# Optimization experiments

Measured on AMD Instinct MI355X. Metric: run time of the kernel, lower is better.

## Reference

```python
import jax, jax.numpy as jnp
import numpy as np

B, C, W, H, Z = 2, 32, 96, 96, 64
IC = C  # inter_channels defaults to in_channels (required by depthwise g conv)
THRESH = 1.5
EPS = 1e-5


def setup_inputs() -> dict:
    key = jax.random.key(0)
    ks = jax.random.split(key, 12)
    s1 = 1.0 / np.sqrt(C)   # 1x1x1 conv fan-in
    s3 = 1.0 / np.sqrt(3.0) # depthwise (1,1,3) conv fan-in per channel
    return {
        "x": jax.random.normal(ks[0], (B, C, W, H, Z), jnp.float32),
        # per-sample spacings in [0,3): mixes both branches around thresh 1.5
        "spacings": jax.random.uniform(ks[1], (B, 3), jnp.float32) * 3.0,
        "theta_w": jax.random.normal(ks[2], (IC, C), jnp.float32) * s1,
        "theta_b": jax.random.normal(ks[3], (IC,), jnp.float32) * s1,
        "phi_w": jax.random.normal(ks[4], (IC, C), jnp.float32) * s1,
        "phi_b": jax.random.normal(ks[5], (IC,), jnp.float32) * s1,
        "g_w": jax.random.normal(ks[6], (C, 3), jnp.float32) * s3,   # depthwise kernel along z
        "g_b": jax.random.normal(ks[7], (C,), jnp.float32) * s3,
        "W_w": jax.random.normal(ks[8], (C, IC), jnp.float32) * s1,
        "W_b": jax.random.normal(ks[9], (C,), jnp.float32) * s1,
        # torch inits BN gamma=0, beta=0 (zero-init residual trick); use small random
        "bn_gamma": jax.random.normal(ks[10], (C,), jnp.float32) * 0.1,
        "bn_beta": jax.random.normal(ks[11], (C,), jnp.float32) * 0.1,
    }


def _cvec(v):
    return v.reshape(1, -1, 1, 1, 1)


def _conv1x1(h, w, b):
    # 1x1x1 Conv3d == channel-mixing matmul
    return jnp.einsum('bcwhz,oc->bowhz', h, w) + _cvec(b)


def reference(x, spacings, theta_w, theta_b, phi_w, phi_b, g_w, g_b, W_w, W_b, bn_gamma, bn_beta):
    # theta/phi: 1x1x1 convs -> (B, IC, W, H, Z)
    t = _conv1x1(x, theta_w, theta_b)
    p = _conv1x1(x, phi_w, phi_b)

    # g: depthwise conv along z, kernel 3, pad 1 (groups=C)
    xp = jnp.pad(x, ((0, 0), (0, 0), (0, 0), (0, 0), (1, 1)))
    gx = (xp[..., :-2] * _cvec(g_w[:, 0])
          + xp[..., 1:-1] * _cvec(g_w[:, 1])
          + xp[..., 2:] * _cvec(g_w[:, 2])
          + _cvec(g_b))

    # non-local attention along z per (b, w, h) row: scores (B, W, H, Z, Z)
    f = jnp.einsum('bcwhz,bcwhy->bwhzy', t, p)
    a = jax.nn.softmax(f, axis=-1)
    y = jnp.einsum('bwhzy,bcwhy->bcwhz', a, gx)
    nl = y + x  # residual inside compute_x

    # per-sample branch on z-spacing, vectorized with where
    mask = (spacings[:, -1] <= THRESH).reshape(-1, 1, 1, 1, 1)
    res = jnp.where(mask, nl, x)

    # W: 1x1x1 conv + BatchNorm3d (training-mode batch stats)
    out = _conv1x1(res, W_w, W_b)
    mean = jnp.mean(out, axis=(0, 2, 3, 4), keepdims=True)
    var = jnp.var(out, axis=(0, 2, 3, 4), keepdims=True)
    out = (out - mean) * jax.lax.rsqrt(var + EPS)
    return out * _cvec(bn_gamma) + _cvec(bn_beta)
```

## Files before the change

kernel.cpp:

```cpp
#include <hip/hip_runtime.h>
#include <stdint.h>

#define CHS 589824
#define ROWS 18432
#define WHn 9216
#define NRED 1179648.0f
#define LOG2E 1.4426950408889634f

typedef short s16x8 __attribute__((ext_vector_type(8)));
typedef float f32x4v __attribute__((ext_vector_type(4)));

#define MFMA16 __builtin_amdgcn_mfma_f32_16x16x32_bf16

#define WSFRAG 10240

#define OXH 0
#define OP  8704
#define OG  13312
#define LDSZ 17664

static __device__ __forceinline__ uint16_t bfh(float v) {
    union { __bf16 h; uint16_t u; } c; c.h = (__bf16)v; return c.u;
}
static __device__ __forceinline__ float bf2f(uint16_t u) {
    union { uint32_t x; float f; } c; c.x = (uint32_t)u << 16; return c.f;
}
static __device__ __forceinline__ uint32_t pk2u(uint16_t a, uint16_t b) {
    return (uint32_t)a | ((uint32_t)b << 16);
}
static __device__ __forceinline__ uint32_t pkbf(float a, float b) {
    return pk2u(bfh(a), bfh(b));
}
static __device__ __forceinline__ float ex2(float x) {
    float r;
    asm("v_exp_f32 %0, %1" : "=v"(r) : "v"(x));
    return r;
}
static __device__ __forceinline__ s16x8 rd8(const char* p) {
    union { uint64_t q[2]; s16x8 s; } v;
    v.q[0] = *(const uint64_t*)p;
    v.q[1] = *(const uint64_t*)(p + 8);
    return v.s;
}

static __device__ __forceinline__ void wfrag2(const float* __restrict__ Wp, int mt, int l15, int kb,
                                              float sc, s16x8& hi, s16x8& lo) {
    const float* p = Wp + (l15 + 16*mt)*32 + 8*kb;
    const float4 f0 = *(const float4*)p;
    const float4 f1 = *(const float4*)(p + 4);
    float f[8] = {f0.x*sc, f0.y*sc, f0.z*sc, f0.w*sc, f1.x*sc, f1.y*sc, f1.z*sc, f1.w*sc};
    union { uint32_t u[4]; s16x8 v; } rh, rl;
    #pragma unroll
    for (int i = 0; i < 4; ++i) {
        const uint16_t h0 = bfh(f[2*i]), h1 = bfh(f[2*i+1]);
        rh.u[i] = pk2u(h0, h1);
        rl.u[i] = pk2u(bfh(f[2*i] - bf2f(h0)), bfh(f[2*i+1] - bf2f(h1)));
    }
    hi = rh.v; lo = rl.v;
}
static __device__ __forceinline__ s16x8 wfragW(const float* __restrict__ Wp, int mt, int l15, int kb) {
    const float* p = Wp + (l15 + 16*mt)*32;
    const float4 f0 = *(const float4*)(p + 4*kb);
    const float4 f1 = *(const float4*)(p + 16 + 4*kb);
    union { uint32_t u[4]; s16x8 v; } r;
    r.u[0] = pkbf(f0.x, f0.y); r.u[1] = pkbf(f0.z, f0.w);
    r.u[2] = pkbf(f1.x, f1.y); r.u[3] = pkbf(f1.z, f1.w);
    return r.v;
}

__global__ __launch_bounds__(256) void k0_frag(
    const float* __restrict__ theta_w, const float* __restrict__ phi_w,
    const float* __restrict__ Ww, char* __restrict__ ws)
{
    const int tid = threadIdx.x;
    const int m = tid >> 7;
    const int r = tid & 127;
    const int mt = r >> 6, l = r & 63;
    s16x8 hi, lo;
    wfrag2(m ? phi_w : theta_w, mt, l & 15, l >> 4, m ? 1.0f : LOG2E, hi, lo);
    *(s16x8*)(ws + m*4096 + (mt*64 + l)*16)        = hi;
    *(s16x8*)(ws + m*4096 + 2048 + (mt*64 + l)*16) = lo;
    if (tid < 128) {
        const int mtw = tid >> 6, lw = tid & 63;
        *(s16x8*)(ws + 8192 + (mtw*64 + lw)*16) = wfragW(Ww, mtw, lw & 15, lw >> 4);
    }
}

__global__ __launch_bounds__(128, 4) void k1_row(
    const float* __restrict__ x, const float* __restrict__ spacings,
    const float* __restrict__ theta_b, const float* __restrict__ phi_b,
    const float* __restrict__ g_w, const float* __restrict__ g_b,
    const float* __restrict__ Wb, const char* __restrict__ frags,
    float* __restrict__ out, float* __restrict__ part)
{
    __shared__ __align__(16) char lds[LDSZ];
    const int t = threadIdx.x;
    const int wv = t >> 6, l = t & 63;
    const int l15 = l & 15, kb = l >> 4;
    const int row = blockIdx.x;
    const int b = row / WHn, wh = row - b*WHn;
    const long base = (long)b*32*CHS + (long)wh*64;

    float xv[16];
    {
        const float* xp = x + base;
        #pragma unroll
        for (int j = 0; j < 16; ++j) xv[j] = xp[(long)(16*wv + j)*CHS + l];
    }
    {
        #pragma unroll
        for (int j = 0; j < 8; ++j) {
            const int c0 = 16*wv + 2*j;
            const uint16_t h0 = bfh(xv[2*j]), h1 = bfh(xv[2*j+1]);
            *(uint32_t*)(lds + OXH + l*136 + c0*2)      = pk2u(h0, h1);
            *(uint32_t*)(lds + OXH + l*136 + 64 + c0*2) =
                pk2u(bfh(xv[2*j] - bf2f(h0)), bfh(xv[2*j+1] - bf2f(h1)));
        }
        const int pG = 32*(l >> 5) + 8*((l >> 2) & 3) + 4*((l >> 4) & 1) + (l & 3);
        #pragma unroll
        for (int j = 0; j < 16; ++j) {
            const int c = 16*wv + j;
            float xm = __shfl_up(xv[j], 1);    if (l == 0)  xm = 0.f;
            float xp2 = __shfl_down(xv[j], 1); if (l == 63) xp2 = 0.f;
            const float g = g_w[3*c]*xm + g_w[3*c+1]*xv[j] + g_w[3*c+2]*xp2 + g_b[c];
            *(uint16_t*)(lds + OG + c*136 + 2*pG) = bfh(g);
        }
    }
    __syncthreads();

    s16x8 bth[2], btl[2];
    {
        s16x8 bxh[2], bxl[2];
        #pragma unroll
        for (int nt = 0; nt < 2; ++nt) {
            const int zr = 32*wv + 16*nt + l15;
            bxh[nt] = rd8(lds + OXH + zr*136 + 16*kb);
            bxl[nt] = rd8(lds + OXH + zr*136 + 64 + 16*kb);
        }
        {
            const s16x8 t0h = *(const s16x8*)(frags + l*16);
            const s16x8 t1h = *(const s16x8*)(frags + 1024 + l*16);
            const s16x8 t0l = *(const s16x8*)(frags + 2048 + l*16);
            const s16x8 t1l = *(const s16x8*)(frags + 3072 + l*16);
            const float4 b0 = *(const float4*)(theta_b + 4*kb);
            const float4 b1 = *(const float4*)(theta_b + 16 + 4*kb);
            #pragma unroll
            for (int nt = 0; nt < 2; ++nt) {
                f32x4v T0; T0[0]=b0.x*LOG2E; T0[1]=b0.y*LOG2E; T0[2]=b0.z*LOG2E; T0[3]=b0.w*LOG2E;
                f32x4v T1; T1[0]=b1.x*LOG2E; T1[1]=b1.y*LOG2E; T1[2]=b1.z*LOG2E; T1[3]=b1.w*LOG2E;
                T0 = MFMA16(t0h, bxh[nt], T0, 0, 0, 0);
                T0 = MFMA16(t0h, bxl[nt], T0, 0, 0, 0);
                T0 = MFMA16(t0l, bxh[nt], T0, 0, 0, 0);
                T1 = MFMA16(t1h, bxh[nt], T1, 0, 0, 0);
                T1 = MFMA16(t1h, bxl[nt], T1, 0, 0, 0);
                T1 = MFMA16(t1l, bxh[nt], T1, 0, 0, 0);
                uint16_t h[8];
                #pragma unroll
                for (int r = 0; r < 4; ++r) { h[r] = bfh(T0[r]); h[4+r] = bfh(T1[r]); }
                union { uint32_t u[4]; s16x8 s; } H, L2;
                H.u[0] = pk2u(h[0], h[1]); H.u[1] = pk2u(h[2], h[3]);
                H.u[2] = pk2u(h[4], h[5]); H.u[3] = pk2u(h[6], h[7]);
                L2.u[0] = pkbf(T0[0]-bf2f(h[0]), T0[1]-bf2f(h[1]));
                L2.u[1] = pkbf(T0[2]-bf2f(h[2]), T0[3]-bf2f(h[3]));
                L2.u[2] = pkbf(T1[0]-bf2f(h[4]), T1[1]-bf2f(h[5]));
                L2.u[3] = pkbf(T1[2]-bf2f(h[6]), T1[3]-bf2f(h[7]));
                bth[nt] = H.s; btl[nt] = L2.s;
            }
        }
        {
            const s16x8 p0h = *(const s16x8*)(frags + 4096 + l*16);
            const s16x8 p1h = *(const s16x8*)(frags + 4096 + 1024 + l*16);
            const s16x8 p0l = *(const s16x8*)(frags + 4096 + 2048 + l*16);
            const s16x8 p1l = *(const s16x8*)(frags + 4096 + 3072 + l*16);
            const float4 c0 = *(const float4*)(phi_b + 4*kb);
            const float4 c1 = *(const float4*)(phi_b + 16 + 4*kb);
            #pragma unroll
            for (int nt = 0; nt < 2; ++nt) {
                const int zr = 32*wv + 16*nt + l15;
                f32x4v P0; P0[0]=c0.x; P0[1]=c0.y; P0[2]=c0.z; P0[3]=c0.w;
                f32x4v P1; P1[0]=c1.x; P1[1]=c1.y; P1[2]=c1.z; P1[3]=c1.w;
                P0 = MFMA16(p0h, bxh[nt], P0, 0, 0, 0);
                P0 = MFMA16(p0h, bxl[nt], P0, 0, 0, 0);
                P0 = MFMA16(p0l, bxh[nt], P0, 0, 0, 0);
                P1 = MFMA16(p1h, bxh[nt], P1, 0, 0, 0);
                P1 = MFMA16(p1h, bxl[nt], P1, 0, 0, 0);
                P1 = MFMA16(p1l, bxh[nt], P1, 0, 0, 0);
                union { uint32_t u[2]; uint64_t q; } w;
                w.u[0] = pkbf(P0[0], P0[1]); w.u[1] = pkbf(P0[2], P0[3]);
                *(uint64_t*)(lds + OP + zr*72 + 16*kb) = w.q;
                w.u[0] = pkbf(P1[0], P1[1]); w.u[1] = pkbf(P1[2], P1[3]);
                *(uint64_t*)(lds + OP + zr*72 + 16*kb + 8) = w.q;
            }
        }
    }
    __syncthreads();

    f32x4v Fq[2][4];
    __builtin_amdgcn_s_setprio(1);
    #pragma unroll
    for (int yt = 0; yt < 4; ++yt) {
        const s16x8 pah = rd8(lds + OP + (16*yt + l15)*72 + 16*kb);
        #pragma unroll
        for (int nt = 0; nt < 2; ++nt) {
            f32x4v zz; zz[0]=0.f; zz[1]=0.f; zz[2]=0.f; zz[3]=0.f;
            zz = MFMA16(pah, bth[nt], zz, 0, 0, 0);
            zz = MFMA16(pah, btl[nt], zz, 0, 0, 0);
            Fq[nt][yt] = zz;
        }
    }
    __builtin_amdgcn_s_setprio(0);

    s16x8 apk[2][2];
    float inv[2];
    #pragma unroll
    for (int nt = 0; nt < 2; ++nt) {
        float mx = -3.4e38f;
        #pragma unroll
        for (int yt = 0; yt < 4; ++yt)
            #pragma unroll
            for (int r = 0; r < 4; ++r) mx = fmaxf(mx, Fq[nt][yt][r]);
        mx = fmaxf(mx, __shfl_xor(mx, 16));
        mx = fmaxf(mx, __shfl_xor(mx, 32));
        float p[4][4]; float sum = 0.f;
        #pragma unroll
        for (int yt = 0; yt < 4; ++yt)
            #pragma unroll
            for (int r = 0; r < 4; ++r) { p[yt][r] = ex2(Fq[nt][yt][r] - mx); sum += p[yt][r]; }
        sum += __shfl_xor(sum, 16);
        sum += __shfl_xor(sum, 32);
        inv[nt] = 1.0f / sum;
        #pragma unroll
        for (int ks = 0; ks < 2; ++ks) {
            union { uint32_t u[4]; s16x8 s; } A;
            A.u[0] = pkbf(p[2*ks][0],   p[2*ks][1]);
            A.u[1] = pkbf(p[2*ks][2],   p[2*ks][3]);
            A.u[2] = pkbf(p[2*ks+1][0], p[2*ks+1][1]);
            A.u[3] = pkbf(p[2*ks+1][2], p[2*ks+1][3]);
            apk[nt][ks] = A.s;
        }
    }

    const bool msk = spacings[b*3 + 2] <= 1.5f;
    s16x8 brf[2];
    #pragma unroll
    for (int nt = 0; nt < 2; ++nt) {
        const int zr = 32*wv + 16*nt + l15;
        f32x4v Yq[2];
        #pragma unroll
        for (int r = 0; r < 4; ++r) { Yq[0][r] = 0.f; Yq[1][r] = 0.f; }
        __builtin_amdgcn_s_setprio(1);
        #pragma unroll
        for (int ks = 0; ks < 2; ++ks) {
            #pragma unroll
            for (int mt = 0; mt < 2; ++mt) {
                const s16x8 gA = rd8(lds + OG + (16*mt + l15)*136 + 64*ks + 16*kb);
                Yq[mt] = MFMA16(gA, apk[nt][ks], Yq[mt], 0, 0, 0);
            }
        }
        __builtin_amdgcn_s_setprio(0);
        union { uint32_t u[4]; s16x8 s; } R;
        #pragma unroll
        for (int mt = 0; mt < 2; ++mt) {
            const uint64_t xh = *(const uint64_t*)(lds + OXH + zr*136 + (16*mt + 4*kb)*2);
            float rv[4];
            #pragma unroll
            for (int r = 0; r < 4; ++r) {
                const float xr = bf2f((uint16_t)(xh >> (16*r)));
                rv[r] = msk ? fmaf(Yq[mt][r], inv[nt], xr) : xr;
            }
            R.u[2*mt]   = pkbf(rv[0], rv[1]);
            R.u[2*mt+1] = pkbf(rv[2], rv[3]);
        }
        brf[nt] = R.s;
    }

    {
        const s16x8 aW0 = *(const s16x8*)(frags + 8192 + l*16);
        const s16x8 aW1 = *(const s16x8*)(frags + 8192 + (64 + l)*16);
        const float4 wb0 = *(const float4*)(Wb + 4*kb);
        const float4 wb1 = *(const float4*)(Wb + 16 + 4*kb);
        #pragma unroll
        for (int nt = 0; nt < 2; ++nt) {
            const int zr = 32*wv + 16*nt + l15;
            f32x4v accs[2];
            f32x4v a0; a0[0]=wb0.x; a0[1]=wb0.y; a0[2]=wb0.z; a0[3]=wb0.w;
            f32x4v a1; a1[0]=wb1.x; a1[1]=wb1.y; a1[2]=wb1.z; a1[3]=wb1.w;
            __builtin_amdgcn_s_setprio(1);
            accs[0] = MFMA16(aW0, brf[nt], a0, 0, 0, 0);
            accs[1] = MFMA16(aW1, brf[nt], a1, 0, 0, 0);
            __builtin_amdgcn_s_setprio(0);
            float* op = out + base + zr;
            #pragma unroll
            for (int mt = 0; mt < 2; ++mt)
                #pragma unroll
                for (int r = 0; r < 4; ++r)
                    op[(long)(16*mt + 4*kb + r)*CHS] = accs[mt][r];
            const int sr = row*4 + 2*wv + nt;
            float bs[8];
            #pragma unroll
            for (int mt = 0; mt < 2; ++mt)
                #pragma unroll
                for (int r = 0; r < 4; ++r) bs[4*mt+r] = accs[mt][r];
            #pragma unroll
            for (int off = 1; off < 16; off <<= 1)
                #pragma unroll
                for (int i = 0; i < 8; ++i) bs[i] += __shfl_xor(bs[i], off);
            if (l15 == 0) {
                #pragma unroll
                for (int mt = 0; mt < 2; ++mt)
                    #pragma unroll
                    for (int r = 0; r < 4; ++r)
                        part[sr*64 + 16*mt + 4*kb + r] = bs[4*mt+r];
            }
            #pragma unroll
            for (int mt = 0; mt < 2; ++mt)
                #pragma unroll
                for (int r = 0; r < 4; ++r) { const float v = accs[mt][r]; bs[4*mt+r] = v*v; }
            #pragma unroll
            for (int off = 1; off < 16; off <<= 1)
                #pragma unroll
                for (int i = 0; i < 8; ++i) bs[i] += __shfl_xor(bs[i], off);
            if (l15 == 0) {
                #pragma unroll
                for (int mt = 0; mt < 2; ++mt)
                    #pragma unroll
                    for (int r = 0; r < 4; ++r)
                        part[sr*64 + 32 + 16*mt + 4*kb + r] = bs[4*mt+r];
            }
        }
    }
}

__global__ __launch_bounds__(256) void k2a(const float* __restrict__ part,
                                           float* __restrict__ part2)
{
    __shared__ float red[4][64];
    const int t = threadIdx.x, lane = t & 63, grp = t >> 6;
    const int p = blockIdx.x;
    float s = 0.f;
    for (int k = 0; k < 72; ++k) s += part[(p*288 + grp + 4*k)*64 + lane];
    red[grp][lane] = s;
    __syncthreads();
    if (t < 64) part2[p*64 + t] = red[0][t] + red[1][t] + red[2][t] + red[3][t];
}

__global__ __launch_bounds__(256) void k2b(const float* __restrict__ part2,
    const float* __restrict__ gamma, const float* __restrict__ beta,
    float* __restrict__ sc)
{
    __shared__ float red[4][64];
    __shared__ float tot[64];
    const int t = threadIdx.x, lane = t & 63, grp = t >> 6;
    float s = 0.f;
    for (int k = 0; k < 64; ++k) s += part2[(grp + 4*k)*64 + lane];
    red[grp][lane] = s;
    __syncthreads();
    if (t < 64) tot[t] = red[0][t] + red[1][t] + red[2][t] + red[3][t];
    __syncthreads();
    if (t < 32) {
        const float mean = tot[t] / NRED;
        const float var  = tot[32+t] / NRED - mean*mean;
        const float rstd = rsqrtf(var + 1e-5f);
        const float scale = gamma[t] * rstd;
        sc[t]    = scale;
        sc[32+t] = fmaf(-mean, scale, beta[t]);
    }
}

__global__ __launch_bounds__(256) void k3_norm(float* __restrict__ out,
                                               const float* __restrict__ sc)
{
    __shared__ float s[64];
    if (threadIdx.x < 64) s[threadIdx.x] = sc[threadIdx.x];
    __syncthreads();
    const int total4 = 2*32*CHS/4;
    const int Q = CHS/4;
    for (int i = blockIdx.x*256 + threadIdx.x; i < total4; i += gridDim.x*256) {
        float4 v = ((const float4*)out)[i];
        const int c = (i / Q) & 31;
        const float scale = s[c], shift = s[32+c];
        v.x = fmaf(v.x, scale, shift);
        v.y = fmaf(v.y, scale, shift);
        v.z = fmaf(v.z, scale, shift);
        v.w = fmaf(v.w, scale, shift);
        ((float4*)out)[i] = v;
    }
}

extern "C" void kernel_launch(void* const* d_in, const int* in_sizes, int n_in,
                              void* d_out, int out_size, void* d_ws, size_t ws_size,
                              hipStream_t stream) {
    const float* x        = (const float*)d_in[0];
    const float* spacings = (const float*)d_in[1];
    const float* theta_w  = (const float*)d_in[2];
    const float* theta_b  = (const float*)d_in[3];
    const float* phi_w    = (const float*)d_in[4];
    const float* phi_b    = (const float*)d_in[5];
    const float* g_w      = (const float*)d_in[6];
    const float* g_b      = (const float*)d_in[7];
    const float* Ww       = (const float*)d_in[8];
    const float* Wb       = (const float*)d_in[9];
    const float* gamma    = (const float*)d_in[10];
    const float* beta     = (const float*)d_in[11];
    float* out   = (float*)d_out;
    char*  frags = (char*)d_ws;
    float* part  = (float*)((char*)d_ws + WSFRAG);
    float* part2 = part + (size_t)ROWS*256;
    float* sc    = part2 + 256*64;

    hipLaunchKernelGGL(k0_frag, dim3(1), dim3(256), 0, stream, theta_w, phi_w, Ww, frags);
    hipLaunchKernelGGL(k1_row, dim3(ROWS), dim3(128), 0, stream,
                       x, spacings, theta_b, phi_b, g_w, g_b, Wb, frags, out, part);
    hipLaunchKernelGGL(k2a, dim3(256), dim3(256), 0, stream, part, part2);
    hipLaunchKernelGGL(k2b, dim3(1), dim3(256), 0, stream, part2, gamma, beta, sc);
    hipLaunchKernelGGL(k3_norm, dim3(4096), dim3(256), 0, stream, out, sc);
}
```

Baseline: 171.8 us.

## Process two rows per block and prefetch the next row's input during compute

The row kernel now handles two consecutive (w,h) rows per block, halving the grid. It loads the second row's x values into registers after the first row's projection stage, so the global load overlaps with the score, softmax and output MFMA work. Per-block setup such as reading the spacing mask is amortized over both rows. The cost is higher register pressure from the extra 16-float buffer, which could reduce occupancy under the (128,4) launch bounds, plus an added barrier between iterations.

```diff
diff --git a/kernel.cpp b/kernel.cpp
--- a/kernel.cpp
+++ b/kernel.cpp
@@ -97,235 +97,243 @@
     const int t = threadIdx.x;
     const int wv = t >> 6, l = t & 63;
     const int l15 = l & 15, kb = l >> 4;
-    const int row = blockIdx.x;
-    const int b = row / WHn, wh = row - b*WHn;
+    const int row0 = blockIdx.x*2;
+    const int b = row0 / WHn, wh = row0 - b*WHn;
     const long base = (long)b*32*CHS + (long)wh*64;
-
-    float xv[16];
-    {
-        const float* xp = x + base;
+    const bool msk = spacings[b*3 + 2] <= 1.5f;
+
+    float xv[2][16];
+    #pragma unroll
+    for (int j = 0; j < 16; ++j) xv[0][j] = x[base + (long)(16*wv + j)*CHS + l];
+
+    #pragma unroll
+    for (int it = 0; it < 2; ++it) {
+        {
+            #pragma unroll
+            for (int j = 0; j < 8; ++j) {
+                const int c0 = 16*wv + 2*j;
+                const uint16_t h0 = bfh(xv[it][2*j]), h1 = bfh(xv[it][2*j+1]);
+                *(uint32_t*)(lds + OXH + l*136 + c0*2)      = pk2u(h0, h1);
+                *(uint32_t*)(lds + OXH + l*136 + 64 + c0*2) =
+                    pk2u(bfh(xv[it][2*j] - bf2f(h0)), bfh(xv[it][2*j+1] - bf2f(h1)));
+            }
+            const int pG = 32*(l >> 5) + 8*((l >> 2) & 3) + 4*((l >> 4) & 1) + (l & 3);
+            #pragma unroll
+            for (int j = 0; j < 16; ++j) {
+                const int c = 16*wv + j;
+                float xm = __shfl_up(xv[it][j], 1);    if (l == 0)  xm = 0.f;
+                float xp2 = __shfl_down(xv[it][j], 1); if (l == 63) xp2 = 0.f;
+                const float g = g_w[3*c]*xm + g_w[3*c+1]*xv[it][j] + g_w[3*c+2]*xp2 + g_b[c];
+                *(uint16_t*)(lds + OG + c*136 + 2*pG) = bfh(g);
+            }
+        }
+        __syncthreads();
+
+        s16x8 bth[2], btl[2];
+        {
+            s16x8 bxh[2], bxl[2];
+            #pragma unroll
+            for (int nt = 0; nt < 2; ++nt) {
+                const int zr = 32*wv + 16*nt + l15;
+                bxh[nt] = rd8(lds + OXH + zr*136 + 16*kb);
+                bxl[nt] = rd8(lds + OXH + zr*136 + 64 + 16*kb);
+            }
+            {
+                const s16x8 t0h = *(const s16x8*)(frags + l*16);
+                const s16x8 t1h = *(const s16x8*)(frags + 1024 + l*16);
+                const s16x8 t0l = *(const s16x8*)(frags + 2048 + l*16);
+                const s16x8 t1l = *(const s16x8*)(frags + 3072 + l*16);
+                const float4 b0 = *(const float4*)(theta_b + 4*kb);
+                const float4 b1 = *(const float4*)(theta_b + 16 + 4*kb);
+                #pragma unroll
+                for (int nt = 0; nt < 2; ++nt) {
+                    f32x4v T0; T0[0]=b0.x*LOG2E; T0[1]=b0.y*LOG2E; T0[2]=b0.z*LOG2E; T0[3]=b0.w*LOG2E;
+                    f32x4v T1; T1[0]=b1.x*LOG2E; T1[1]=b1.y*LOG2E; T1[2]=b1.z*LOG2E; T1[3]=b1.w*LOG2E;
+                    T0 = MFMA16(t0h, bxh[nt], T0, 0, 0, 0);
+                    T0 = MFMA16(t0h, bxl[nt], T0, 0, 0, 0);
+                    T0 = MFMA16(t0l, bxh[nt], T0, 0, 0, 0);
+                    T1 = MFMA16(t1h, bxh[nt], T1, 0, 0, 0);
+                    T1 = MFMA16(t1h, bxl[nt], T1, 0, 0, 0);
+                    T1 = MFMA16(t1l, bxh[nt], T1, 0, 0, 0);
+                    uint16_t h[8];
+                    #pragma unroll
+                    for (int r = 0; r < 4; ++r) { h[r] = bfh(T0[r]); h[4+r] = bfh(T1[r]); }
+                    union { uint32_t u[4]; s16x8 s; } H, L2;
+                    H.u[0] = pk2u(h[0], h[1]); H.u[1] = pk2u(h[2], h[3]);
+                    H.u[2] = pk2u(h[4], h[5]); H.u[3] = pk2u(h[6], h[7]);
+                    L2.u[0] = pkbf(T0[0]-bf2f(h[0]), T0[1]-bf2f(h[1]));
+                    L2.u[1] = pkbf(T0[2]-bf2f(h[2]), T0[3]-bf2f(h[3]));
+                    L2.u[2] = pkbf(T1[0]-bf2f(h[4]), T1[1]-bf2f(h[5]));
+                    L2.u[3] = pkbf(T1[2]-bf2f(h[6]), T1[3]-bf2f(h[7]));
+                    bth[nt] = H.s; btl[nt] = L2.s;
+                }
+            }
+            {
+                const s16x8 p0h = *(const s16x8*)(frags + 4096 + l*16);
+                const s16x8 p1h = *(const s16x8*)(frags + 4096 + 1024 + l*16);
+                const s16x8 p0l = *(const s16x8*)(frags + 4096 + 2048 + l*16);
+                const s16x8 p1l = *(const s16x8*)(frags + 4096 + 3072 + l*16);
+                const float4 c0 = *(const float4*)(phi_b + 4*kb);
+                const float4 c1 = *(const float4*)(phi_b + 16 + 4*kb);
+                #pragma unroll
+                for (int nt = 0; nt < 2; ++nt) {
+                    const int zr = 32*wv + 16*nt + l15;
+                    f32x4v P0; P0[0]=c0.x; P0[1]=c0.y; P0[2]=c0.z; P0[3]=c0.w;
+                    f32x4v P1; P1[0]=c1.x; P1[1]=c1.y; P1[2]=c1.z; P1[3]=c1.w;
+                    P0 = MFMA16(p0h, bxh[nt], P0, 0, 0, 0);
+                    P0 = MFMA16(p0h, bxl[nt], P0, 0, 0, 0);
+                    P0 = MFMA16(p0l, bxh[nt], P0, 0, 0, 0);
+                    P1 = MFMA16(p1h, bxh[nt], P1, 0, 0, 0);
+                    P1 = MFMA16(p1h, bxl[nt], P1, 0, 0, 0);
+                    P1 = MFMA16(p1l, bxh[nt], P1, 0, 0, 0);
+                    union { uint32_t u[2]; uint64_t q; } w;
+                    w.u[0] = pkbf(P0[0], P0[1]); w.u[1] = pkbf(P0[2], P0[3]);
+                    *(uint64_t*)(lds + OP + zr*72 + 16*kb) = w.q;
+                    w.u[0] = pkbf(P1[0], P1[1]); w.u[1] = pkbf(P1[2], P1[3]);
+                    *(uint64_t*)(lds + OP + zr*72 + 16*kb + 8) = w.q;
+                }
+            }
+        }
+        __syncthreads();
+
+        if (it == 0) {
+            #pragma unroll
+            for (int j = 0; j < 16; ++j)
+                xv[1][j] = x[base + 64 + (long)(16*wv + j)*CHS + l];
+        }
+
+        f32x4v Fq[2][4];
+        __builtin_amdgcn_s_setprio(1);
         #pragma unroll
-        for (int j = 0; j < 16; ++j) xv[j] = xp[(long)(16*wv + j)*CHS + l];
-    }
-    {
+        for (int yt = 0; yt < 4; ++yt) {
+            const s16x8 pah = rd8(lds + OP + (16*yt + l15)*72 + 16*kb);
+            #pragma unroll
+            for (int nt = 0; nt < 2; ++nt) {
+                f32x4v zz; zz[0]=0.f; zz[1]=0.f; zz[2]=0.f; zz[3]=0.f;
+                zz = MFMA16(pah, bth[nt], zz, 0, 0, 0);
+                zz = MFMA16(pah, btl[nt], zz, 0, 0, 0);
+                Fq[nt][yt] = zz;
+            }
+        }
+        __builtin_amdgcn_s_setprio(0);
+
+        s16x8 apk[2][2];
+        float inv[2];
         #pragma unroll
-        for (int j = 0; j < 8; ++j) {
-            const int c0 = 16*wv + 2*j;
-            const uint16_t h0 = bfh(xv[2*j]), h1 = bfh(xv[2*j+1]);
-            *(uint32_t*)(lds + OXH + l*136 + c0*2)      = pk2u(h0, h1);
-            *(uint32_t*)(lds + OXH + l*136 + 64 + c0*2) =
-                pk2u(bfh(xv[2*j] - bf2f(h0)), bfh(xv[2*j+1] - bf2f(h1)));
-        }
-        const int pG = 32*(l >> 5) + 8*((l >> 2) & 3) + 4*((l >> 4) & 1) + (l & 3);
-        #pragma unroll
-        for (int j = 0; j < 16; ++j) {
-            const int c = 16*wv + j;
-            float xm = __shfl_up(xv[j], 1);    if (l == 0)  xm = 0.f;
-            float xp2 = __shfl_down(xv[j], 1); if (l == 63) xp2 = 0.f;
-            const float g = g_w[3*c]*xm + g_w[3*c+1]*xv[j] + g_w[3*c+2]*xp2 + g_b[c];
-            *(uint16_t*)(lds + OG + c*136 + 2*pG) = bfh(g);
-        }
-    }
-    __syncthreads();
-
-    s16x8 bth[2], btl[2];
-    {
-        s16x8 bxh[2], bxl[2];
+        for (int nt = 0; nt < 2; ++nt) {
+            float mx = -3.4e38f;
+            #pragma unroll
+            for (int yt = 0; yt < 4; ++yt)
+                #pragma unroll
+                for (int r = 0; r < 4; ++r) mx = fmaxf(mx, Fq[nt][yt][r]);
+            mx = fmaxf(mx, __shfl_xor(mx, 16));
+            mx = fmaxf(mx, __shfl_xor(mx, 32));
+            float p[4][4]; float sum = 0.f;
+            #pragma unroll
+            for (int yt = 0; yt < 4; ++yt)
+                #pragma unroll
+                for (int r = 0; r < 4; ++r) { p[yt][r] = ex2(Fq[nt][yt][r] - mx); sum += p[yt][r]; }
+            sum += __shfl_xor(sum, 16);
+            sum += __shfl_xor(sum, 32);
+            inv[nt] = 1.0f / sum;
+            #pragma unroll
+            for (int ks = 0; ks < 2; ++ks) {
+                union { uint32_t u[4]; s16x8 s; } A;
+                A.u[0] = pkbf(p[2*ks][0],   p[2*ks][1]);
+                A.u[1] = pkbf(p[2*ks][2],   p[2*ks][3]);
+                A.u[2] = pkbf(p[2*ks+1][0], p[2*ks+1][1]);
+                A.u[3] = pkbf(p[2*ks+1][2], p[2*ks+1][3]);
+                apk[nt][ks] = A.s;
+            }
+        }
+
+        s16x8 brf[2];
         #pragma unroll
         for (int nt = 0; nt < 2; ++nt) {
             const int zr = 32*wv + 16*nt + l15;
-            bxh[nt] = rd8(lds + OXH + zr*136 + 16*kb);
-            bxl[nt] = rd8(lds + OXH + zr*136 + 64 + 16*kb);
-        }
+            f32x4v Yq[2];
+            #pragma unroll
+            for (int r = 0; r < 4; ++r) { Yq[0][r] = 0.f; Yq[1][r] = 0.f; }
+            __builtin_amdgcn_s_setprio(1);
+            #pragma unroll
+            for (int ks = 0; ks < 2; ++ks) {
+                #pragma unroll
+                for (int mt = 0; mt < 2; ++mt) {
+                    const s16x8 gA = rd8(lds + OG + (16*mt + l15)*136 + 64*ks + 16*kb);
+                    Yq[mt] = MFMA16(gA, apk[nt][ks], Yq[mt], 0, 0, 0);
+                }
+            }
+            __builtin_amdgcn_s_setprio(0);
+            union { uint32_t u[4]; s16x8 s; } R;
+            #pragma unroll
+            for (int mt = 0; mt < 2; ++mt) {
+                const uint64_t xh = *(const uint64_t*)(lds + OXH + zr*136 + (16*mt + 4*kb)*2);
+                float rv[4];
+                #pragma unroll
+                for (int r = 0; r < 4; ++r) {
+                    const float xr = bf2f((uint16_t)(xh >> (16*r)));
+                    rv[r] = msk ? fmaf(Yq[mt][r], inv[nt], xr) : xr;
+                }
+                R.u[2*mt]   = pkbf(rv[0], rv[1]);
+                R.u[2*mt+1] = pkbf(rv[2], rv[3]);
+            }
+            brf[nt] = R.s;
+        }
+        if (it == 0) __syncthreads();
+
         {
-            const s16x8 t0h = *(const s16x8*)(frags + l*16);
-            const s16x8 t1h = *(const s16x8*)(frags + 1024 + l*16);
-            const s16x8 t0l = *(const s16x8*)(frags + 2048 + l*16);
-            const s16x8 t1l = *(const s16x8*)(frags + 3072 + l*16);
-            const float4 b0 = *(const float4*)(theta_b + 4*kb);
-            const float4 b1 = *(const float4*)(theta_b + 16 + 4*kb);
-            #pragma unroll
-            for (int nt = 0; nt < 2; ++nt) {
-                f32x4v T0; T0[0]=b0.x*LOG2E; T0[1]=b0.y*LOG2E; T0[2]=b0.z*LOG2E; T0[3]=b0.w*LOG2E;
-                f32x4v T1; T1[0]=b1.x*LOG2E; T1[1]=b1.y*LOG2E; T1[2]=b1.z*LOG2E; T1[3]=b1.w*LOG2E;
-                T0 = MFMA16(t0h, bxh[nt], T0, 0, 0, 0);
-                T0 = MFMA16(t0h, bxl[nt], T0, 0, 0, 0);
-                T0 = MFMA16(t0l, bxh[nt], T0, 0, 0, 0);
-                T1 = MFMA16(t1h, bxh[nt], T1, 0, 0, 0);
-                T1 = MFMA16(t1h, bxl[nt], T1, 0, 0, 0);
-                T1 = MFMA16(t1l, bxh[nt], T1, 0, 0, 0);
-                uint16_t h[8];
-                #pragma unroll
-                for (int r = 0; r < 4; ++r) { h[r] = bfh(T0[r]); h[4+r] = bfh(T1[r]); }
-                union { uint32_t u[4]; s16x8 s; } H, L2;
-                H.u[0] = pk2u(h[0], h[1]); H.u[1] = pk2u(h[2], h[3]);
-                H.u[2] = pk2u(h[4], h[5]); H.u[3] = pk2u(h[6], h[7]);
-                L2.u[0] = pkbf(T0[0]-bf2f(h[0]), T0[1]-bf2f(h[1]));
-                L2.u[1] = pkbf(T0[2]-bf2f(h[2]), T0[3]-bf2f(h[3]));
-                L2.u[2] = pkbf(T1[0]-bf2f(h[4]), T1[1]-bf2f(h[5]));
-                L2.u[3] = pkbf(T1[2]-bf2f(h[6]), T1[3]-bf2f(h[7]));
-                bth[nt] = H.s; btl[nt] = L2.s;
-            }
-        }
-        {
-            const s16x8 p0h = *(const s16x8*)(frags + 4096 + l*16);
-            const s16x8 p1h = *(const s16x8*)(frags + 4096 + 1024 + l*16);
-            const s16x8 p0l = *(const s16x8*)(frags + 4096 + 2048 + l*16);
-            const s16x8 p1l = *(const s16x8*)(frags + 4096 + 3072 + l*16);
-            const float4 c0 = *(const float4*)(phi_b + 4*kb);
-            const float4 c1 = *(const float4*)(phi_b + 16 + 4*kb);
+            const s16x8 aW0 = *(const s16x8*)(frags + 8192 + l*16);
+            const s16x8 aW1 = *(const s16x8*)(frags + 8192 + (64 + l)*16);
+            const float4 wb0 = *(const float4*)(Wb + 4*kb);
+            const float4 wb1 = *(const float4*)(Wb + 16 + 4*kb);
             #pragma unroll
             for (int nt = 0; nt < 2; ++nt) {
                 const int zr = 32*wv + 16*nt + l15;
-                f32x4v P0; P0[0]=c0.x; P0[1]=c0.y; P0[2]=c0.z; P0[3]=c0.w;
-                f32x4v P1; P1[0]=c1.x; P1[1]=c1.y; P1[2]=c1.z; P1[3]=c1.w;
-                P0 = MFMA16(p0h, bxh[nt], P0, 0, 0, 0);
-                P0 = MFMA16(p0h, bxl[nt], P0, 0, 0, 0);
-                P0 = MFMA16(p0l, bxh[nt], P0, 0, 0, 0);
-                P1 = MFMA16(p1h, bxh[nt], P1, 0, 0, 0);
-                P1 = MFMA16(p1h, bxl[nt], P1, 0, 0, 0);
-                P1 = MFMA16(p1l, bxh[nt], P1, 0, 0, 0);
-                union { uint32_t u[2]; uint64_t q; } w;
-                w.u[0] = pkbf(P0[0], P0[1]); w.u[1] = pkbf(P0[2], P0[3]);
-                *(uint64_t*)(lds + OP + zr*72 + 16*kb) = w.q;
-                w.u[0] = pkbf(P1[0], P1[1]); w.u[1] = pkbf(P1[2], P1[3]);
-                *(uint64_t*)(lds + OP + zr*72 + 16*kb + 8) = w.q;
-            }
-        }
-    }
-    __syncthreads();
-
-    f32x4v Fq[2][4];
-    __builtin_amdgcn_s_setprio(1);
-    #pragma unroll
-    for (int yt = 0; yt < 4; ++yt) {
-        const s16x8 pah = rd8(lds + OP + (16*yt + l15)*72 + 16*kb);
-        #pragma unroll
-        for (int nt = 0; nt < 2; ++nt) {
-            f32x4v zz; zz[0]=0.f; zz[1]=0.f; zz[2]=0.f; zz[3]=0.f;
-            zz = MFMA16(pah, bth[nt], zz, 0, 0, 0);
-            zz = MFMA16(pah, btl[nt], zz, 0, 0, 0);
-            Fq[nt][yt] = zz;
-        }
-    }
-    __builtin_amdgcn_s_setprio(0);
-
-    s16x8 apk[2][2];
-    float inv[2];
-    #pragma unroll
-    for (int nt = 0; nt < 2; ++nt) {
-        float mx = -3.4e38f;
-        #pragma unroll
-        for (int yt = 0; yt < 4; ++yt)
-            #pragma unroll
-            for (int r = 0; r < 4; ++r) mx = fmaxf(mx, Fq[nt][yt][r]);
-        mx = fmaxf(mx, __shfl_xor(mx, 16));
-        mx = fmaxf(mx, __shfl_xor(mx, 32));
-        float p[4][4]; float sum = 0.f;
-        #pragma unroll
-        for (int yt = 0; yt < 4; ++yt)
-            #pragma unroll
-            for (int r = 0; r < 4; ++r) { p[yt][r] = ex2(Fq[nt][yt][r] - mx); sum += p[yt][r]; }
-        sum += __shfl_xor(sum, 16);
-        sum += __shfl_xor(sum, 32);
-        inv[nt] = 1.0f / sum;
-        #pragma unroll
-        for (int ks = 0; ks < 2; ++ks) {
-            union { uint32_t u[4]; s16x8 s; } A;
-            A.u[0] = pkbf(p[2*ks][0],   p[2*ks][1]);
-            A.u[1] = pkbf(p[2*ks][2],   p[2*ks][3]);
-            A.u[2] = pkbf(p[2*ks+1][0], p[2*ks+1][1]);
-            A.u[3] = pkbf(p[2*ks+1][2], p[2*ks+1][3]);
-            apk[nt][ks] = A.s;
-        }
-    }
-
-    const bool msk = spacings[b*3 + 2] <= 1.5f;
-    s16x8 brf[2];
-    #pragma unroll
-    for (int nt = 0; nt < 2; ++nt) {
-        const int zr = 32*wv + 16*nt + l15;
-        f32x4v Yq[2];
-        #pragma unroll
-        for (int r = 0; r < 4; ++r) { Yq[0][r] = 0.f; Yq[1][r] = 0.f; }
-        __builtin_amdgcn_s_setprio(1);
-        #pragma unroll
-        for (int ks = 0; ks < 2; ++ks) {
-            #pragma unroll
-            for (int mt = 0; mt < 2; ++mt) {
-                const s16x8 gA = rd8(lds + OG + (16*mt + l15)*136 + 64*ks + 16*kb);
-                Yq[mt] = MFMA16(gA, apk[nt][ks], Yq[mt], 0, 0, 0);
-            }
-        }
-        __builtin_amdgcn_s_setprio(0);
-        union { uint32_t u[4]; s16x8 s; } R;
-        #pragma unroll
-        for (int mt = 0; mt < 2; ++mt) {
-            const uint64_t xh = *(const uint64_t*)(lds + OXH + zr*136 + (16*mt + 4*kb)*2);
-            float rv[4];
-            #pragma unroll
-            for (int r = 0; r < 4; ++r) {
-                const float xr = bf2f((uint16_t)(xh >> (16*r)));
-                rv[r] = msk ? fmaf(Yq[mt][r], inv[nt], xr) : xr;
-            }
-            R.u[2*mt]   = pkbf(rv[0], rv[1]);
-            R.u[2*mt+1] = pkbf(rv[2], rv[3]);
-        }
-        brf[nt] = R.s;
-    }
-
-    {
-        const s16x8 aW0 = *(const s16x8*)(frags + 8192 + l*16);
-        const s16x8 aW1 = *(const s16x8*)(frags + 8192 + (64 + l)*16);
-        const float4 wb0 = *(const float4*)(Wb + 4*kb);
-        const float4 wb1 = *(const float4*)(Wb + 16 + 4*kb);
-        #pragma unroll
-        for (int nt = 0; nt < 2; ++nt) {
-            const int zr = 32*wv + 16*nt + l15;
-            f32x4v accs[2];
-            f32x4v a0; a0[0]=wb0.x; a0[1]=wb0.y; a0[2]=wb0.z; a0[3]=wb0.w;
-            f32x4v a1; a1[0]=wb1.x; a1[1]=wb1.y; a1[2]=wb1.z; a1[3]=wb1.w;
-            __builtin_amdgcn_s_setprio(1);
-            accs[0] = MFMA16(aW0, brf[nt], a0, 0, 0, 0);
-            accs[1] = MFMA16(aW1, brf[nt], a1, 0, 0, 0);
-            __builtin_amdgcn_s_setprio(0);
-            float* op = out + base + zr;
-            #pragma unroll
-            for (int mt = 0; mt < 2; ++mt)
-                #pragma unroll
-                for (int r = 0; r < 4; ++r)
-                    op[(long)(16*mt + 4*kb + r)*CHS] = accs[mt][r];
-            const int sr = row*4 + 2*wv + nt;
-            float bs[8];
-            #pragma unroll
-            for (int mt = 0; mt < 2; ++mt)
-                #pragma unroll
-                for (int r = 0; r < 4; ++r) bs[4*mt+r] = accs[mt][r];
-            #pragma unroll
-            for (int off = 1; off < 16; off <<= 1)
-                #pragma unroll
-                for (int i = 0; i < 8; ++i) bs[i] += __shfl_xor(bs[i], off);
-            if (l15 == 0) {
+                f32x4v accs[2];
+                f32x4v a0; a0[0]=wb0.x; a0[1]=wb0.y; a0[2]=wb0.z; a0[3]=wb0.w;
+                f32x4v a1; a1[0]=wb1.x; a1[1]=wb1.y; a1[2]=wb1.z; a1[3]=wb1.w;
+                __builtin_amdgcn_s_setprio(1);
+                accs[0] = MFMA16(aW0, brf[nt], a0, 0, 0, 0);
+                accs[1] = MFMA16(aW1, brf[nt], a1, 0, 0, 0);
+                __builtin_amdgcn_s_setprio(0);
+                float* op = out + base + it*64 + zr;
                 #pragma unroll
                 for (int mt = 0; mt < 2; ++mt)
                     #pragma unroll
                     for (int r = 0; r < 4; ++r)
-                        part[sr*64 + 16*mt + 4*kb + r] = bs[4*mt+r];
-            }
-            #pragma unroll
-            for (int mt = 0; mt < 2; ++mt)
-                #pragma unroll
-                for (int r = 0; r < 4; ++r) { const float v = accs[mt][r]; bs[4*mt+r] = v*v; }
-            #pragma unroll
-            for (int off = 1; off < 16; off <<= 1)
-                #pragma unroll
-                for (int i = 0; i < 8; ++i) bs[i] += __shfl_xor(bs[i], off);
-            if (l15 == 0) {
+                        op[(long)(16*mt + 4*kb + r)*CHS] = accs[mt][r];
+                const int sr = (row0 + it)*4 + 2*wv + nt;
+                float bs[8];
                 #pragma unroll
                 for (int mt = 0; mt < 2; ++mt)
                     #pragma unroll
-                    for (int r = 0; r < 4; ++r)
-                        part[sr*64 + 32 + 16*mt + 4*kb + r] = bs[4*mt+r];
+                    for (int r = 0; r < 4; ++r) bs[4*mt+r] = accs[mt][r];
+                #pragma unroll
+                for (int off = 1; off < 16; off <<= 1)
+                    #pragma unroll
+                    for (int i = 0; i < 8; ++i) bs[i] += __shfl_xor(bs[i], off);
+                if (l15 == 0) {
+                    #pragma unroll
+                    for (int mt = 0; mt < 2; ++mt)
+                        #pragma unroll
+                        for (int r = 0; r < 4; ++r)
+                            part[sr*64 + 16*mt + 4*kb + r] = bs[4*mt+r];
+                }
+                #pragma unroll
+                for (int mt = 0; mt < 2; ++mt)
+                    #pragma unroll
+                    for (int r = 0; r < 4; ++r) { const float v = accs[mt][r]; bs[4*mt+r] = v*v; }
+                #pragma unroll
+                for (int off = 1; off < 16; off <<= 1)
+                    #pragma unroll
+                    for (int i = 0; i < 8; ++i) bs[i] += __shfl_xor(bs[i], off);
+                if (l15 == 0) {
+                    #pragma unroll
+                    for (int mt = 0; mt < 2; ++mt)
+                        #pragma unroll
+                        for (int r = 0; r < 4; ++r)
+                            part[sr*64 + 32 + 16*mt + 4*kb + r] = bs[4*mt+r];
+                }
             }
         }
     }
@@ -409,7 +417,7 @@
     float* sc    = part2 + 256*64;
 
     hipLaunchKernelGGL(k0_frag, dim3(1), dim3(256), 0, stream, theta_w, phi_w, Ww, frags);
-    hipLaunchKernelGGL(k1_row, dim3(ROWS), dim3(128), 0, stream,
+    hipLaunchKernelGGL(k1_row, dim3(ROWS/2), dim3(128), 0, stream,
                        x, spacings, theta_b, phi_b, g_w, g_b, Wb, frags, out, part);
     hipLaunchKernelGGL(k2a, dim3(256), dim3(256), 0, stream, part, part2);
     hipLaunchKernelGGL(k2b, dim3(1), dim3(256), 0, stream, part2, gamma, beta, sc);
```

After: 207.8 us. 1.21x slower.
